# Kernel tuning notes

Hardware: AMD Instinct MI355X
Metric: run time of the kernel (lower is better)

Reference implementation:

```python
import jax, jax.numpy as jnp
import numpy as np

D_MODEL = 1024
HID = 4096  # d_model * att_size
N_KEYS = 65536
TOP_K = 6


def setup_inputs() -> dict:
    root = jax.random.key(0)
    k0, k1, k2, k3, k4, k5 = jax.random.split(root, 6)
    s = 1.0 / np.sqrt(D_MODEL)
    return {
        "query": jax.random.normal(k0, (D_MODEL,), dtype=jnp.float32),
        "key_mat": jax.random.normal(k1, (N_KEYS, D_MODEL), dtype=jnp.float32),
        "Wq": jax.random.normal(k2, (HID, D_MODEL), dtype=jnp.float32) * s,
        "bq": jax.random.normal(k3, (HID,), dtype=jnp.float32) * s,
        "Wk": jax.random.normal(k4, (HID, D_MODEL), dtype=jnp.float32) * s,
        "bk": jax.random.normal(k5, (HID,), dtype=jnp.float32) * s,
    }


def reference(query, key_mat, Wq, bq, Wk, bk):
    # Linear projections (nn.Linear: x @ W^T + b)
    q = jnp.dot(Wq, query) + bq                 # [HID]
    k = jnp.dot(key_mat, Wk.T) + bk             # [N, HID]
    scores = jnp.dot(k, q)                      # [N]
    # The torch loop does k=6 sequential argmax + mask(-100000) + gather,
    # which (absent pathological -100000 scores) is exactly top-6 selection.
    _, idx = jax.lax.top_k(scores, TOP_K)       # [TOP_K]
    return jnp.mean(key_mat[idx], axis=0)       # [D_MODEL]
```

## Files before the change

### kernel.cpp

```cpp
#include <hip/hip_runtime.h>

#define DM    1024
#define HID   4096
#define NKEYS 65536
#define TOPK  6
#define NEGF  (-3.4e38f)

typedef float fvec4 __attribute__((ext_vector_type(4)));

__device__ __forceinline__ fvec4 nt_load4(const float* p) {
    return __builtin_nontemporal_load((const fvec4*)p);
}

__global__ __launch_bounds__(256) void proj_fused_kernel(const float* __restrict__ Wq,
                                                         const float* __restrict__ query,
                                                         const float* __restrict__ bq,
                                                         const float* __restrict__ Wk,
                                                         float* __restrict__ v_part) {
    const int t = threadIdx.x, b = blockIdx.x;
    const int wave = t >> 6, lane = t & 63;
    const int h0 = b * 16;
    __shared__ float qs[16];

    const fvec4* __restrict__ qv = (const fvec4*)query;
#pragma unroll
    for (int j = 0; j < 4; ++j) {
        const int h = h0 + wave * 4 + j;
        const float* Wrow = Wq + (size_t)h * DM;
        float acc = 0.f;
#pragma unroll
        for (int k = 0; k < 4; ++k) {
            fvec4 w = nt_load4(Wrow + (lane + k * 64) * 4);
            fvec4 x = qv[lane + k * 64];
            acc += w.x * x.x + w.y * x.y + w.z * x.z + w.w * x.w;
        }
#pragma unroll
        for (int off = 32; off > 0; off >>= 1) acc += __shfl_down(acc, off);
        if (lane == 0) qs[wave * 4 + j] = acc + bq[h];
    }
    __syncthreads();

    fvec4 acc4 = {0.f, 0.f, 0.f, 0.f};
#pragma unroll 4
    for (int j = 0; j < 16; ++j) {
        fvec4 w = nt_load4(Wk + (size_t)(h0 + j) * DM + t * 4);
        acc4 += w * qs[j];
    }
    *(fvec4*)(v_part + (size_t)b * DM + t * 4) = acc4;
}

__global__ __launch_bounds__(64) void vreduce_kernel(const float* __restrict__ v_part,
                                                     float* __restrict__ v) {
    const int d = blockIdx.x * 64 + threadIdx.x;
    float acc = 0.f;
#pragma unroll 8
    for (int b = 0; b < 256; ++b) acc += v_part[(size_t)b * DM + d];
    v[d] = acc;
}

__global__ __launch_bounds__(256) void score_kernel(const float* __restrict__ key_mat,
                                                    const float* __restrict__ v,
                                                    float* __restrict__ scores) {
    const int wave = threadIdx.x >> 6;
    const int lane = threadIdx.x & 63;
    const int r = blockIdx.x * 4 + wave;
    const float* row = key_mat + (size_t)r * DM;
    const fvec4* __restrict__ vv = (const fvec4*)v;
    float acc = 0.f;
#pragma unroll
    for (int k = 0; k < 4; ++k) {
        fvec4 a = nt_load4(row + (lane + k * 64) * 4);
        fvec4 b = vv[lane + k * 64];
        acc += a.x * b.x + a.y * b.y + a.z * b.z + a.w * b.w;
    }
#pragma unroll
    for (int off = 32; off > 0; off >>= 1) acc += __shfl_down(acc, off);
    if (lane == 0) scores[r] = acc;
}

__global__ __launch_bounds__(256) void topk_stage1(const float* __restrict__ scores,
                                                   float* __restrict__ cand_v,
                                                   int* __restrict__ cand_i) {
    const int t = threadIdx.x, b = blockIdx.x;
    const int i = b * 256 + t;
    float cur = scores[i];

    __shared__ float wv[4];
    __shared__ int   wi[4];
    __shared__ float selv[TOPK];
    __shared__ int   seli[TOPK];

    for (int p = 0; p < TOPK; ++p) {
        float m = cur; int mi = i;
#pragma unroll
        for (int off = 32; off > 0; off >>= 1) {
            float ov = __shfl_down(m, off);
            int   oi = __shfl_down(mi, off);
            if (ov > m) { m = ov; mi = oi; }
        }
        const int lane = t & 63, w = t >> 6;
        if (lane == 0) { wv[w] = m; wi[w] = mi; }
        __syncthreads();
        if (t == 0) {
            float bm = wv[0]; int bix = wi[0];
#pragma unroll
            for (int j = 1; j < 4; ++j) if (wv[j] > bm) { bm = wv[j]; bix = wi[j]; }
            selv[p] = bm; seli[p] = bix;
        }
        __syncthreads();
        if (i == seli[p]) cur = NEGF;
    }
    if (t < TOPK) { cand_v[b * TOPK + t] = selv[t]; cand_i[b * TOPK + t] = seli[t]; }
}

__global__ __launch_bounds__(256) void topk_stage2_mean(const float* __restrict__ cand_v,
                                                        const int* __restrict__ cand_i,
                                                        const float* __restrict__ key_mat,
                                                        float* __restrict__ out) {
    const int t = threadIdx.x;
    const int NC = 256 * TOPK;

    __shared__ float sv[NC];
    __shared__ int   si[NC];
    __shared__ float wv[4];
    __shared__ int   wi[4];
    __shared__ int   sel[TOPK];

#pragma unroll
    for (int j = 0; j < TOPK; ++j) {
        sv[t + j * 256] = cand_v[t + j * 256];
        si[t + j * 256] = cand_i[t + j * 256];
    }
    __syncthreads();

    for (int p = 0; p < TOPK; ++p) {
        float m = NEGF; int mp = 0;
#pragma unroll
        for (int j = 0; j < TOPK; ++j) {
            const int pos = t * TOPK + j;
            const float val = sv[pos];
            if (val > m) { m = val; mp = pos; }
        }
#pragma unroll
        for (int off = 32; off > 0; off >>= 1) {
            float ov = __shfl_down(m, off);
            int   op = __shfl_down(mp, off);
            if (ov > m) { m = ov; mp = op; }
        }
        const int lane = t & 63, w = t >> 6;
        if (lane == 0) { wv[w] = m; wi[w] = mp; }
        __syncthreads();
        if (t == 0) {
            float bm = wv[0]; int bp = wi[0];
#pragma unroll
            for (int j = 1; j < 4; ++j) if (wv[j] > bm) { bm = wv[j]; bp = wi[j]; }
            sel[p] = si[bp];
            sv[bp] = NEGF;
        }
        __syncthreads();
    }

    fvec4 acc = {0.f, 0.f, 0.f, 0.f};
#pragma unroll
    for (int p = 0; p < TOPK; ++p)
        acc += *(const fvec4*)(key_mat + (size_t)sel[p] * DM + t * 4);
    acc *= (1.0f / 6.0f);
    *(fvec4*)(out + t * 4) = acc;
}

extern "C" void kernel_launch(void* const* d_in, const int* in_sizes, int n_in,
                              void* d_out, int out_size, void* d_ws, size_t ws_size,
                              hipStream_t stream) {
    const float* query   = (const float*)d_in[0];
    const float* key_mat = (const float*)d_in[1];
    const float* Wq      = (const float*)d_in[2];
    const float* bq      = (const float*)d_in[3];
    const float* Wk      = (const float*)d_in[4];
    float* out = (float*)d_out;

    float* ws      = (float*)d_ws;
    float* v_part  = ws;
    float* v       = v_part + 256 * DM;
    float* scores  = v + DM;
    float* cand_v  = scores + NKEYS;
    int*   cand_i  = (int*)(cand_v + 256 * TOPK);

    proj_fused_kernel<<<256,       256, 0, stream>>>(Wq, query, bq, Wk, v_part);
    vreduce_kernel   <<<DM / 64,   64,  0, stream>>>(v_part, v);
    score_kernel     <<<NKEYS / 4, 256, 0, stream>>>(key_mat, v, scores);
    topk_stage1      <<<256,       256, 0, stream>>>(scores, cand_v, cand_i);
    topk_stage2_mean <<<1,         256, 0, stream>>>(cand_v, cand_i, key_mat, out);
}
```

Measured before the change: 381.2 us.

## Fuse score computation with per-block top-k and widen vector reduce

Scoring and the first top-k stage are merged into one kernel. Each of 2048 blocks scores 32 rows, keeping the score vector in registers, and selects its local top-6 within a single wave, so the global scores array and one launch go away. The vector reduce now splits the 256 partials across four waves per block, and the query vector is hoisted into registers in the projection kernel. The second stage now has to scan 12288 candidates instead of 1536 in a single block, which adds serial work at the end.

```diff
diff --git a/kernel.cpp b/kernel.cpp
--- a/kernel.cpp
+++ b/kernel.cpp
@@ -5,6 +5,11 @@
 #define NKEYS 65536
 #define TOPK  6
 #define NEGF  (-3.4e38f)
+
+#define SBLK  2048
+#define RPB   (NKEYS / SBLK)
+#define RPW   (RPB / 4)
+#define NC    (SBLK * TOPK)
 
 typedef float fvec4 __attribute__((ext_vector_type(4)));
 
@@ -23,6 +28,10 @@
     __shared__ float qs[16];
 
     const fvec4* __restrict__ qv = (const fvec4*)query;
+    fvec4 xq[4];
+#pragma unroll
+    for (int k = 0; k < 4; ++k) xq[k] = qv[lane + k * 64];
+
 #pragma unroll
     for (int j = 0; j < 4; ++j) {
         const int h = h0 + wave * 4 + j;
@@ -31,8 +40,7 @@
 #pragma unroll
         for (int k = 0; k < 4; ++k) {
             fvec4 w = nt_load4(Wrow + (lane + k * 64) * 4);
-            fvec4 x = qv[lane + k * 64];
-            acc += w.x * x.x + w.y * x.y + w.z * x.z + w.w * x.w;
+            acc += w.x * xq[k].x + w.y * xq[k].y + w.z * xq[k].z + w.w * xq[k].w;
         }
 #pragma unroll
         for (int off = 32; off > 0; off >>= 1) acc += __shfl_down(acc, off);
@@ -49,68 +57,68 @@
     *(fvec4*)(v_part + (size_t)b * DM + t * 4) = acc4;
 }
 
-__global__ __launch_bounds__(64) void vreduce_kernel(const float* __restrict__ v_part,
-                                                     float* __restrict__ v) {
-    const int d = blockIdx.x * 64 + threadIdx.x;
+__global__ __launch_bounds__(256) void vreduce_kernel(const float* __restrict__ v_part,
+                                                      float* __restrict__ v) {
+    const int t = threadIdx.x, w = t >> 6, lane = t & 63;
+    const int d = blockIdx.x * 64 + lane;
+    __shared__ float part[4][64];
     float acc = 0.f;
 #pragma unroll 8
-    for (int b = 0; b < 256; ++b) acc += v_part[(size_t)b * DM + d];
-    v[d] = acc;
+    for (int b = w * 64; b < w * 64 + 64; ++b) acc += v_part[(size_t)b * DM + d];
+    part[w][lane] = acc;
+    __syncthreads();
+    if (w == 0) v[d] = part[0][lane] + part[1][lane] + part[2][lane] + part[3][lane];
 }
 
-__global__ __launch_bounds__(256) void score_kernel(const float* __restrict__ key_mat,
-                                                    const float* __restrict__ v,
-                                                    float* __restrict__ scores) {
-    const int wave = threadIdx.x >> 6;
-    const int lane = threadIdx.x & 63;
-    const int r = blockIdx.x * 4 + wave;
-    const float* row = key_mat + (size_t)r * DM;
+__global__ __launch_bounds__(256) void score_topk1_kernel(const float* __restrict__ key_mat,
+                                                          const float* __restrict__ v,
+                                                          float* __restrict__ cand_v,
+                                                          int* __restrict__ cand_i) {
+    const int t = threadIdx.x, b = blockIdx.x;
+    const int wave = t >> 6, lane = t & 63;
+    const int r0 = b * RPB + wave * RPW;
+
+    __shared__ float sc[RPB];
+
     const fvec4* __restrict__ vv = (const fvec4*)v;
-    float acc = 0.f;
+    fvec4 vb[4];
 #pragma unroll
-    for (int k = 0; k < 4; ++k) {
-        fvec4 a = nt_load4(row + (lane + k * 64) * 4);
-        fvec4 b = vv[lane + k * 64];
-        acc += a.x * b.x + a.y * b.y + a.z * b.z + a.w * b.w;
+    for (int k = 0; k < 4; ++k) vb[k] = vv[lane + k * 64];
+
+#pragma unroll
+    for (int j = 0; j < RPW; ++j) {
+        const float* row = key_mat + (size_t)(r0 + j) * DM;
+        float acc = 0.f;
+#pragma unroll
+        for (int k = 0; k < 4; ++k) {
+            fvec4 a = nt_load4(row + (lane + k * 64) * 4);
+            acc += a.x * vb[k].x + a.y * vb[k].y + a.z * vb[k].z + a.w * vb[k].w;
+        }
+#pragma unroll
+        for (int off = 32; off > 0; off >>= 1) acc += __shfl_down(acc, off);
+        if (lane == 0) sc[wave * RPW + j] = acc;
     }
+    __syncthreads();
+
+    if (wave == 0) {
+        float val = (lane < RPB) ? sc[lane] : NEGF;
 #pragma unroll
-    for (int off = 32; off > 0; off >>= 1) acc += __shfl_down(acc, off);
-    if (lane == 0) scores[r] = acc;
-}
-
-__global__ __launch_bounds__(256) void topk_stage1(const float* __restrict__ scores,
-                                                   float* __restrict__ cand_v,
-                                                   int* __restrict__ cand_i) {
-    const int t = threadIdx.x, b = blockIdx.x;
-    const int i = b * 256 + t;
-    float cur = scores[i];
-
-    __shared__ float wv[4];
-    __shared__ int   wi[4];
-    __shared__ float selv[TOPK];
-    __shared__ int   seli[TOPK];
-
-    for (int p = 0; p < TOPK; ++p) {
-        float m = cur; int mi = i;
+        for (int p = 0; p < TOPK; ++p) {
+            float m = val; int ml = lane;
 #pragma unroll
-        for (int off = 32; off > 0; off >>= 1) {
-            float ov = __shfl_down(m, off);
-            int   oi = __shfl_down(mi, off);
-            if (ov > m) { m = ov; mi = oi; }
+            for (int off = 32; off > 0; off >>= 1) {
+                float ov = __shfl_down(m, off);
+                int   ol = __shfl_down(ml, off);
+                if (ov > m) { m = ov; ml = ol; }
+            }
+            if (lane == 0) {
+                cand_v[b * TOPK + p] = m;
+                cand_i[b * TOPK + p] = b * RPB + ml;
+            }
+            ml = __shfl(ml, 0);
+            if (lane == ml) val = NEGF;
         }
-        const int lane = t & 63, w = t >> 6;
-        if (lane == 0) { wv[w] = m; wi[w] = mi; }
-        __syncthreads();
-        if (t == 0) {
-            float bm = wv[0]; int bix = wi[0];
-#pragma unroll
-            for (int j = 1; j < 4; ++j) if (wv[j] > bm) { bm = wv[j]; bix = wi[j]; }
-            selv[p] = bm; seli[p] = bix;
-        }
-        __syncthreads();
-        if (i == seli[p]) cur = NEGF;
     }
-    if (t < TOPK) { cand_v[b * TOPK + t] = selv[t]; cand_i[b * TOPK + t] = seli[t]; }
 }
 
 __global__ __launch_bounds__(256) void topk_stage2_mean(const float* __restrict__ cand_v,
@@ -118,26 +126,21 @@
                                                         const float* __restrict__ key_mat,
                                                         float* __restrict__ out) {
     const int t = threadIdx.x;
-    const int NC = 256 * TOPK;
 
     __shared__ float sv[NC];
-    __shared__ int   si[NC];
     __shared__ float wv[4];
     __shared__ int   wi[4];
     __shared__ int   sel[TOPK];
 
 #pragma unroll
-    for (int j = 0; j < TOPK; ++j) {
-        sv[t + j * 256] = cand_v[t + j * 256];
-        si[t + j * 256] = cand_i[t + j * 256];
-    }
+    for (int j = 0; j < NC / 256; ++j) sv[j * 256 + t] = cand_v[j * 256 + t];
     __syncthreads();
 
     for (int p = 0; p < TOPK; ++p) {
         float m = NEGF; int mp = 0;
 #pragma unroll
-        for (int j = 0; j < TOPK; ++j) {
-            const int pos = t * TOPK + j;
+        for (int j = 0; j < NC / 256; ++j) {
+            const int pos = j * 256 + t;
             const float val = sv[pos];
             if (val > m) { m = val; mp = pos; }
         }
@@ -154,7 +157,7 @@
             float bm = wv[0]; int bp = wi[0];
 #pragma unroll
             for (int j = 1; j < 4; ++j) if (wv[j] > bm) { bm = wv[j]; bp = wi[j]; }
-            sel[p] = si[bp];
+            sel[p] = cand_i[bp];
             sv[bp] = NEGF;
         }
         __syncthreads();
@@ -181,13 +184,11 @@
     float* ws      = (float*)d_ws;
     float* v_part  = ws;
     float* v       = v_part + 256 * DM;
-    float* scores  = v + DM;
-    float* cand_v  = scores + NKEYS;
-    int*   cand_i  = (int*)(cand_v + 256 * TOPK);
+    float* cand_v  = v + DM;
+    int*   cand_i  = (int*)(cand_v + NC);
 
-    proj_fused_kernel<<<256,       256, 0, stream>>>(Wq, query, bq, Wk, v_part);
-    vreduce_kernel   <<<DM / 64,   64,  0, stream>>>(v_part, v);
-    score_kernel     <<<NKEYS / 4, 256, 0, stream>>>(key_mat, v, scores);
-    topk_stage1      <<<256,       256, 0, stream>>>(scores, cand_v, cand_i);
-    topk_stage2_mean <<<1,         256, 0, stream>>>(cand_v, cand_i, key_mat, out);
+    proj_fused_kernel <<<256,  256, 0, stream>>>(Wq, query, bq, Wk, v_part);
+    vreduce_kernel    <<<16,   256, 0, stream>>>(v_part, v);
+    score_topk1_kernel<<<SBLK, 256, 0, stream>>>(key_mat, v, cand_v, cand_i);
+    topk_stage2_mean  <<<1,    256, 0, stream>>>(cand_v, cand_i, key_mat, out);
 }
```

Measured after the change: 380.2 us. About the same (-0.3%).
